# Kernel optimization log

Hardware: AMD Instinct MI355X
Metric: run time of the kernel (lower is better)

Reference implementation:

```python
import jax, jax.numpy as jnp
import numpy as np

B, IN_DIM, HID, LAT, L, K = 65536, 512, 256, 64, 3, 2048


def setup_inputs() -> dict:
    key = jax.random.key(0)
    ks = jax.random.split(key, 10)
    s = 0.05
    return {
        "x": jax.random.normal(ks[0], (B, IN_DIM), jnp.float32),
        "enc_w1": jax.random.normal(ks[1], (IN_DIM, HID), jnp.float32) * s,
        "enc_b1": jnp.zeros((HID,), jnp.float32),
        "enc_w2": jax.random.normal(ks[2], (HID, LAT), jnp.float32) * s,
        "enc_b2": jnp.zeros((LAT,), jnp.float32),
        "codebooks": jax.random.normal(ks[3], (L, K, LAT), jnp.float32),
        "dec_w1": jax.random.normal(ks[4], (LAT, HID), jnp.float32) * s,
        "dec_b1": jnp.zeros((HID,), jnp.float32),
        "dec_w2": jax.random.normal(ks[5], (HID, IN_DIM), jnp.float32) * s,
        "dec_b2": jnp.zeros((IN_DIM,), jnp.float32),
    }


def reference(x, enc_w1, enc_b1, enc_w2, enc_b2, codebooks,
              dec_w1, dec_b1, dec_w2, dec_b2):
    # encoder: Linear -> ReLU -> Linear
    z = jax.nn.relu(x @ enc_w1 + enc_b1) @ enc_w2 + enc_b2  # [B, LAT]

    quantized = jnp.zeros_like(z)
    codes, residuals = [], []
    num_layers = codebooks.shape[0]
    for i in range(num_layers):  # small fixed layer loop (structurally sequential)
        residual = z - jax.lax.stop_gradient(quantized)  # [B, LAT]
        residuals.append(residual)
        C = codebooks[i]  # [K, LAT]
        # squared euclidean distances (argmin identical to cdist argmin)
        sqdist = (jnp.sum(residual * residual, axis=-1, keepdims=True)
                  - 2.0 * (residual @ C.T)
                  + jnp.sum(C * C, axis=-1))  # [B, K]
        code = jnp.argmin(sqdist, axis=-1)  # [B]
        codes.append(code)
        quantized = C[code] + jax.lax.stop_gradient(quantized)

    # decoder: Linear -> ReLU -> Linear
    x_recon = jax.nn.relu(quantized @ dec_w1 + dec_b1) @ dec_w2 + dec_b2  # [B, IN_DIM]
    return (jnp.stack(codes), x_recon, quantized, jnp.stack(residuals))
```

## Files before the change

kernel.cpp:

```cpp
#include <hip/hip_runtime.h>
#include <float.h>

#define NB      65536
#define IN_DIM  512
#define HID     256
#define LAT     64
#define NLAYERS 3
#define NK      2048
#define DELTA   1e-2f

typedef __attribute__((ext_vector_type(8)))  short s16x8;
typedef __attribute__((ext_vector_type(16))) float fp32x16;

__device__ __forceinline__ unsigned short f2bf(float v) {
  unsigned u = __float_as_uint(v);
  unsigned r = (u + 0x7fffu + ((u >> 16) & 1u)) >> 16;
  return (unsigned short)r;
}
__device__ __forceinline__ float bf2f(unsigned short h) {
  return __uint_as_float((unsigned)h << 16);
}

template<bool RELU>
__global__ __launch_bounds__(256) void gemm_f32(
    const float* __restrict__ A, const float* __restrict__ W,
    const float* __restrict__ bias, float* __restrict__ C,
    int M, int N, int K) {
  __shared__ float As[32][132];
  __shared__ float Bs[32][64];
  const int tid = threadIdx.x;
  const int cg  = tid & 15;
  const int rg  = tid >> 4;
  const int m0  = blockIdx.x * 128;
  const int n0  = blockIdx.y * 64;

  float acc[8][4];
#pragma unroll
  for (int i = 0; i < 8; ++i)
#pragma unroll
    for (int j = 0; j < 4; ++j) acc[i][j] = 0.f;

  for (int k0 = 0; k0 < K; k0 += 32) {
#pragma unroll
    for (int p = 0; p < 4; ++p) {
      int a = tid + p * 256;
      int row = a >> 3, kq = (a & 7) * 4;
      float4 v = *reinterpret_cast<const float4*>(&A[(size_t)(m0 + row) * K + k0 + kq]);
      As[kq + 0][row] = v.x; As[kq + 1][row] = v.y;
      As[kq + 2][row] = v.z; As[kq + 3][row] = v.w;
    }
#pragma unroll
    for (int p = 0; p < 2; ++p) {
      int a = tid + p * 256;
      int kk = a >> 4, nq = (a & 15) * 4;
      *reinterpret_cast<float4*>(&Bs[kk][nq]) =
          *reinterpret_cast<const float4*>(&W[(size_t)(k0 + kk) * N + n0 + nq]);
    }
    __syncthreads();
#pragma unroll
    for (int kk = 0; kk < 32; ++kk) {
      float4 a0 = *reinterpret_cast<const float4*>(&As[kk][rg * 8]);
      float4 a1 = *reinterpret_cast<const float4*>(&As[kk][rg * 8 + 4]);
      float4 b0 = *reinterpret_cast<const float4*>(&Bs[kk][cg * 4]);
      float av[8] = {a0.x, a0.y, a0.z, a0.w, a1.x, a1.y, a1.z, a1.w};
      float bv[4] = {b0.x, b0.y, b0.z, b0.w};
#pragma unroll
      for (int i = 0; i < 8; ++i)
#pragma unroll
        for (int j = 0; j < 4; ++j)
          acc[i][j] = fmaf(av[i], bv[j], acc[i][j]);
    }
    __syncthreads();
  }

  float4 bb = *reinterpret_cast<const float4*>(&bias[n0 + cg * 4]);
  float bv[4] = {bb.x, bb.y, bb.z, bb.w};
#pragma unroll
  for (int i = 0; i < 8; ++i) {
    float vals[4];
#pragma unroll
    for (int j = 0; j < 4; ++j) {
      float v = __fadd_rn(acc[i][j], bv[j]);
      if (RELU) v = fmaxf(v, 0.f);
      vals[j] = v;
    }
    float4 o; o.x = vals[0]; o.y = vals[1]; o.z = vals[2]; o.w = vals[3];
    *reinterpret_cast<float4*>(&C[(size_t)(m0 + rg * 8 + i) * N + n0 + cg * 4]) = o;
  }
}

template<bool RELU>
__global__ __launch_bounds__(256) void gemm128(
    const float* __restrict__ A, const float* __restrict__ W,
    const float* __restrict__ bias, float* __restrict__ C,
    int M, int N, int K) {
  __shared__ float As[16][132];
  __shared__ float Bs[16][132];
  const int tid  = threadIdx.x;
  const int cg   = tid & 15;
  const int rg   = tid >> 4;
  const int sw   = (cg >> 2) & 1;
  const int colA = cg * 8 + sw * 4;
  const int colB = cg * 8 + (sw ^ 1) * 4;
  const int m0   = blockIdx.x * 128;
  const int n0   = blockIdx.y * 128;

  const int arow = tid >> 2;
  const int akq  = (tid & 3) * 4;
  const int bk   = tid >> 5;
  const int bn   = (tid & 31) * 4;

  const float* Ap0 = A + (size_t)(m0 + arow) * K + akq;
  const float* Ap1 = A + (size_t)(m0 + arow + 64) * K + akq;
  const float* Wp0 = W + (size_t)bk * N + n0 + bn;
  const float* Wp1 = W + (size_t)(bk + 8) * N + n0 + bn;

  float acc[8][8];
#pragma unroll
  for (int i = 0; i < 8; ++i)
#pragma unroll
    for (int j = 0; j < 8; ++j) acc[i][j] = 0.f;

  float4 av0, av1, bv0, bv1;
  av0 = *reinterpret_cast<const float4*>(Ap0);
  av1 = *reinterpret_cast<const float4*>(Ap1);
  bv0 = *reinterpret_cast<const float4*>(Wp0);
  bv1 = *reinterpret_cast<const float4*>(Wp1);

  auto write_tile = [&]() {
    As[akq + 0][arow] = av0.x; As[akq + 1][arow] = av0.y;
    As[akq + 2][arow] = av0.z; As[akq + 3][arow] = av0.w;
    As[akq + 0][arow + 64] = av1.x; As[akq + 1][arow + 64] = av1.y;
    As[akq + 2][arow + 64] = av1.z; As[akq + 3][arow + 64] = av1.w;
    *reinterpret_cast<float4*>(&Bs[bk][bn])     = bv0;
    *reinterpret_cast<float4*>(&Bs[bk + 8][bn]) = bv1;
  };
  auto compute_tile = [&]() {
#pragma unroll
    for (int kk = 0; kk < 16; ++kk) {
      float4 a0 = *reinterpret_cast<const float4*>(&As[kk][rg * 8]);
      float4 a1 = *reinterpret_cast<const float4*>(&As[kk][rg * 8 + 4]);
      float4 b0 = *reinterpret_cast<const float4*>(&Bs[kk][colA]);
      float4 b1 = *reinterpret_cast<const float4*>(&Bs[kk][colB]);
      float rv[8] = {a0.x, a0.y, a0.z, a0.w, a1.x, a1.y, a1.z, a1.w};
      float cv[8] = {b0.x, b0.y, b0.z, b0.w, b1.x, b1.y, b1.z, b1.w};
#pragma unroll
      for (int i = 0; i < 8; ++i)
#pragma unroll
        for (int j = 0; j < 8; ++j)
          acc[i][j] = fmaf(rv[i], cv[j], acc[i][j]);
    }
  };

  write_tile();
  __syncthreads();
#pragma unroll 1
  for (int k0 = 16; k0 < K; k0 += 16) {
    av0 = *reinterpret_cast<const float4*>(Ap0 + k0);
    av1 = *reinterpret_cast<const float4*>(Ap1 + k0);
    bv0 = *reinterpret_cast<const float4*>(Wp0 + (size_t)k0 * N);
    bv1 = *reinterpret_cast<const float4*>(Wp1 + (size_t)k0 * N);
    compute_tile();
    __syncthreads();
    write_tile();
    __syncthreads();
  }
  compute_tile();

  float4 bA = *reinterpret_cast<const float4*>(&bias[n0 + colA]);
  float4 bB = *reinterpret_cast<const float4*>(&bias[n0 + colB]);
  float ba[8] = {bA.x, bA.y, bA.z, bA.w, bB.x, bB.y, bB.z, bB.w};
#pragma unroll
  for (int i = 0; i < 8; ++i) {
    size_t row = (size_t)(m0 + rg * 8 + i);
    float o[8];
#pragma unroll
    for (int j = 0; j < 8; ++j) {
      float v = __fadd_rn(acc[i][j], ba[j]);
      if (RELU) v = fmaxf(v, 0.f);
      o[j] = v;
    }
    float4 oA; oA.x = o[0]; oA.y = o[1]; oA.z = o[2]; oA.w = o[3];
    float4 oB; oB.x = o[4]; oB.y = o[5]; oB.z = o[6]; oB.w = o[7];
    *reinterpret_cast<float4*>(&C[row * N + n0 + colA]) = oA;
    *reinterpret_cast<float4*>(&C[row * N + n0 + colB]) = oB;
  }
}

__global__ void cnorm_f32(const float* __restrict__ cb, float* __restrict__ cn) {
  int i = blockIdx.x * blockDim.x + threadIdx.x;
  if (i >= NLAYERS * NK) return;
  const float* row = cb + (size_t)i * LAT;
  float r[8];
#pragma unroll
  for (int j = 0; j < 8; ++j) r[j] = 0.f;
#pragma unroll
  for (int t = 0; t < 8; ++t)
#pragma unroll
    for (int j = 0; j < 8; ++j) {
      float v = row[t * 8 + j];
      r[j] = __fadd_rn(r[j], __fmul_rn(v, v));
    }
  cn[i] = __fadd_rn(__fadd_rn(__fadd_rn(r[0], r[1]), __fadd_rn(r[2], r[3])),
                    __fadd_rn(__fadd_rn(r[4], r[5]), __fadd_rn(r[6], r[7])));
}

__global__ void split_cb(const float* __restrict__ cb,
                         unsigned short* __restrict__ cbf) {
  const int sid  = blockIdx.x * 256 + threadIdx.x;
  const int lane = sid & 63;
  const int grp  = sid >> 6;
  const int fg   = grp & 7;
  const int chl  = grp >> 3;
  const int nt = fg >> 2, ks = fg & 3;
  const int layer = chl >> 5, ch = chl & 31;
  const int code = ch * 64 + nt * 32 + (lane & 31);
  const int k0 = ks * 16 + (lane >> 5) * 8;
  const float* src = cb + ((size_t)layer * NK + code) * LAT + k0;
  float4 a = *(const float4*)src;
  float4 b = *(const float4*)(src + 4);
  float v[8] = {a.x, a.y, a.z, a.w, b.x, b.y, b.z, b.w};
  s16x8 hi, lo;
#pragma unroll
  for (int i = 0; i < 8; ++i) {
    float nv = __fmul_rn(-2.f, v[i]);
    unsigned short h = f2bf(nv);
    hi[i] = (short)h;
    lo[i] = (short)f2bf(__fsub_rn(nv, bf2f(h)));
  }
  *(s16x8*)(cbf + ((size_t)grp * 2 + 0) * 512 + lane * 8) = hi;
  *(s16x8*)(cbf + ((size_t)grp * 2 + 1) * 512 + lane * 8) = lo;
}

__global__ void split_w(const float* __restrict__ W,
                        unsigned short* __restrict__ wf, int K, int N) {
  const int total = (K / 16) * (N / 32) * 64;
  const int idx = blockIdx.x * 256 + threadIdx.x;
  if (idx >= total) return;
  const int lane = idx & 63;
  const int grp  = idx >> 6;
  const int ntn  = N / 32;
  const int ks   = grp / ntn;
  const int ntg  = grp % ntn;
  const int col  = ntg * 32 + (lane & 31);
  const int k0   = ks * 16 + (lane >> 5) * 8;
  s16x8 hi, lo;
#pragma unroll
  for (int i = 0; i < 8; ++i) {
    float v = W[(size_t)(k0 + i) * N + col];
    unsigned short h = f2bf(v);
    hi[i] = (short)h;
    lo[i] = (short)f2bf(__fsub_rn(v, bf2f(h)));
  }
  *(s16x8*)(wf + ((size_t)grp * 2 + 0) * 512 + lane * 8) = hi;
  *(s16x8*)(wf + ((size_t)grp * 2 + 1) * 512 + lane * 8) = lo;
}

__global__ __launch_bounds__(256, 2) void rq_mfma(
    const float* __restrict__ zg,
    const float* __restrict__ cb,
    const unsigned short* __restrict__ cbf,
    const float* __restrict__ cnorm,
    float* __restrict__ out_codes,
    float* __restrict__ out_quant,
    float* __restrict__ out_res) {
  __shared__ float m1S[128][2];
  __shared__ int   candS[128][8];
  __shared__ int   cntS[128][2];
  __shared__ int   flagS[128][2];
  __shared__ int   selS[128];
  __shared__ float rnS[128];
  __shared__ float bestD[256];
  __shared__ int   bestK[256];

  const int tid   = threadIdx.x;
  const int w     = tid >> 6;
  const int rgrp  = w >> 1;
  const int chalf = w & 1;
  const int lane  = tid & 63;
  const int half  = lane >> 5;
  const int lcol  = lane & 31;
  const int rb0   = blockIdx.x * 128;

  s16x8 ah[2][4], al[2][4];

  for (int layer = 0; layer < NLAYERS; ++layer) {
    const float* cbL = cb + (size_t)layer * NK * LAT;
    const float* cnL = cnorm + (size_t)layer * NK;
    const unsigned short* cbfL = cbf + (size_t)layer * (NK * LAT * 2);
    float* resL = out_res + (size_t)layer * NB * LAT;

#pragma unroll
    for (int m = 0; m < 2; ++m) {
      const size_t row = (size_t)(rb0 + rgrp * 64 + m * 32 + lcol);
#pragma unroll
      for (int ks = 0; ks < 4; ++ks) {
        const int k0 = ks * 16 + half * 8;
        const float* zp = zg + row * LAT + k0;
        float4 a = *(const float4*)zp;
        float4 b = *(const float4*)(zp + 4);
        float r[8] = {a.x, a.y, a.z, a.w, b.x, b.y, b.z, b.w};
        if (layer > 0) {
          const float* qp = out_quant + row * LAT + k0;
          float4 qa = *(const float4*)qp;
          float4 qb = *(const float4*)(qp + 4);
          float q[8] = {qa.x, qa.y, qa.z, qa.w, qb.x, qb.y, qb.z, qb.w};
#pragma unroll
          for (int i = 0; i < 8; ++i) r[i] = __fsub_rn(r[i], q[i]);
          if (chalf == 0) {
            float4 o0 = {r[0], r[1], r[2], r[3]};
            float4 o1 = {r[4], r[5], r[6], r[7]};
            *(float4*)(resL + row * LAT + k0) = o0;
            *(float4*)(resL + row * LAT + k0 + 4) = o1;
          }
        }
#pragma unroll
        for (int i = 0; i < 8; ++i) {
          unsigned short hh = f2bf(r[i]);
          float hf = bf2f(hh);
          ah[m][ks][i] = (short)hh;
          al[m][ks][i] = (short)f2bf(__fsub_rn(r[i], hf));
        }
      }
    }
    __syncthreads();

    if (tid < 128) {
      const float* rp = resL + (size_t)(rb0 + tid) * LAT;
      float r8[8] = {0.f, 0.f, 0.f, 0.f, 0.f, 0.f, 0.f, 0.f};
#pragma unroll
      for (int tb = 0; tb < 8; ++tb) {
        float4 x0 = *(const float4*)(rp + tb * 8);
        float4 x1 = *(const float4*)(rp + tb * 8 + 4);
        float v[8] = {x0.x, x0.y, x0.z, x0.w, x1.x, x1.y, x1.z, x1.w};
#pragma unroll
        for (int j = 0; j < 8; ++j)
          r8[j] = __fadd_rn(r8[j], __fmul_rn(v[j], v[j]));
      }
      rnS[tid] = __fadd_rn(
          __fadd_rn(__fadd_rn(r8[0], r8[1]), __fadd_rn(r8[2], r8[3])),
          __fadd_rn(__fadd_rn(r8[4], r8[5]), __fadd_rn(r8[6], r8[7])));
    }
    __syncthreads();

    float v1[2][16], v2[2][16];
    int   i1[2][16];
#pragma unroll
    for (int m = 0; m < 2; ++m)
#pragma unroll
      for (int r = 0; r < 16; ++r) {
        v1[m][r] = FLT_MAX; v2[m][r] = FLT_MAX; i1[m][r] = 0;
      }

#pragma unroll 1
    for (int ch = 0; ch < 16; ++ch) {
      const int chg = chalf * 16 + ch;
      const unsigned short* cf = cbfL + (size_t)chg * 8192;
#pragma unroll
      for (int nt = 0; nt < 2; ++nt) {
        const int kbase = chg * 64 + nt * 32 + lcol;
        const float cnv = cnL[kbase];
        s16x8 bh[4], bl[4];
#pragma unroll
        for (int ks = 0; ks < 4; ++ks) {
          bh[ks] = *(const s16x8*)(cf + ((size_t)((nt * 4 + ks) * 2 + 0) * 64 + lane) * 8);
          bl[ks] = *(const s16x8*)(cf + ((size_t)((nt * 4 + ks) * 2 + 1) * 64 + lane) * 8);
        }
        fp32x16 acc0, acc1;
#pragma unroll
        for (int r = 0; r < 16; ++r) { acc0[r] = 0.f; acc1[r] = 0.f; }
#pragma unroll
        for (int ks = 0; ks < 4; ++ks) {
          acc0 = __builtin_amdgcn_mfma_f32_32x32x16_bf16(ah[0][ks], bh[ks], acc0, 0, 0, 0);
          acc1 = __builtin_amdgcn_mfma_f32_32x32x16_bf16(ah[1][ks], bh[ks], acc1, 0, 0, 0);
          acc0 = __builtin_amdgcn_mfma_f32_32x32x16_bf16(ah[0][ks], bl[ks], acc0, 0, 0, 0);
          acc1 = __builtin_amdgcn_mfma_f32_32x32x16_bf16(ah[1][ks], bl[ks], acc1, 0, 0, 0);
          acc0 = __builtin_amdgcn_mfma_f32_32x32x16_bf16(al[0][ks], bh[ks], acc0, 0, 0, 0);
          acc1 = __builtin_amdgcn_mfma_f32_32x32x16_bf16(al[1][ks], bh[ks], acc1, 0, 0, 0);
        }
#pragma unroll
        for (int r = 0; r < 16; ++r) {
          {
            float d = __fadd_rn(cnv, acc0[r]);
            v2[0][r] = __builtin_amdgcn_fmed3f(d, v1[0][r], v2[0][r]);
            bool c = d < v1[0][r];
            i1[0][r] = c ? kbase : i1[0][r];
            v1[0][r] = fminf(v1[0][r], d);
          }
          {
            float d = __fadd_rn(cnv, acc1[r]);
            v2[1][r] = __builtin_amdgcn_fmed3f(d, v1[1][r], v2[1][r]);
            bool c = d < v1[1][r];
            i1[1][r] = c ? kbase : i1[1][r];
            v1[1][r] = fminf(v1[1][r], d);
          }
        }
      }
    }

#pragma unroll
    for (int m = 0; m < 2; ++m)
#pragma unroll
      for (int r = 0; r < 16; ++r) {
        float m1 = v1[m][r];
        m1 = fminf(m1, __shfl_xor(m1, 1));
        m1 = fminf(m1, __shfl_xor(m1, 2));
        m1 = fminf(m1, __shfl_xor(m1, 4));
        m1 = fminf(m1, __shfl_xor(m1, 8));
        m1 = fminf(m1, __shfl_xor(m1, 16));
        const int rowloc = rgrp * 64 + m * 32 + (r & 3) + 8 * (r >> 2) + 4 * half;
        if (lcol == 0) m1S[rowloc][chalf] = m1;
      }
    __syncthreads();
#pragma unroll
    for (int m = 0; m < 2; ++m)
#pragma unroll
      for (int r = 0; r < 16; ++r) {
        const int rowloc = rgrp * 64 + m * 32 + (r & 3) + 8 * (r >> 2) + 4 * half;
        float thr = fminf(m1S[rowloc][0], m1S[rowloc][1]) + DELTA;
        unsigned long long bc = __ballot(v1[m][r] <= thr);
        unsigned long long bf = __ballot(v2[m][r] <= thr);
        unsigned mc = (unsigned)(bc >> (half * 32));
        unsigned mf = (unsigned)(bf >> (half * 32));
        int pos = __popc(mc & ((1u << lcol) - 1u));
        if (v1[m][r] <= thr && pos < 4) candS[rowloc][chalf * 4 + pos] = i1[m][r];
        if (lcol == 0) {
          int c = __popc(mc);
          cntS[rowloc][chalf]  = (c < 4) ? c : 4;
          flagS[rowloc][chalf] = (mf != 0u) || (c > 4);
        }
      }
    __syncthreads();

    if (tid < 128) {
      const int t = tid;
      if ((flagS[t][0] | flagS[t][1]) == 0) {
        const float* rp = resL + (size_t)(rb0 + t) * LAT;
        float rr[64];
#pragma unroll
        for (int j = 0; j < 16; ++j) {
          float4 x = *(const float4*)(rp + j * 4);
          rr[j * 4 + 0] = x.x; rr[j * 4 + 1] = x.y;
          rr[j * 4 + 2] = x.z; rr[j * 4 + 3] = x.w;
        }
        const float rn = rnS[t];
        float bd = FLT_MAX; int bk = 0x7fffffff;
        const int c0 = cntS[t][0], c1n = cntS[t][1];
        for (int c = 0; c < c0 + c1n; ++c) {
          int k = candS[t][(c < c0) ? c : (4 + c - c0)];
          const float* cp = cbL + (size_t)k * LAT;
          float dot = 0.f;
#pragma unroll
          for (int j = 0; j < 64; ++j) dot = fmaf(rr[j], cp[j], dot);
          float d = __fadd_rn(__fsub_rn(rn, __fmul_rn(2.f, dot)), cnL[k]);
          if (d < bd || (d == bd && k < bk)) { bd = d; bk = k; }
        }
        selS[t] = bk;
        out_codes[(size_t)layer * NB + rb0 + t] = (float)bk;
      }
    }
    __syncthreads();

#pragma unroll 1
    for (int t2 = 0; t2 < 128; ++t2) {
      if ((flagS[t2][0] | flagS[t2][1]) == 0) continue;
      const float* rp = resL + (size_t)(rb0 + t2) * LAT;
      const float rn = rnS[t2];
      float bd = FLT_MAX; int bk = 0x7fffffff;
#pragma unroll 1
      for (int j = 0; j < 8; ++j) {
        int k = tid * 8 + j;
        const float* cp = cbL + (size_t)k * LAT;
        float dot = 0.f;
        for (int q = 0; q < 64; ++q) dot = fmaf(rp[q], cp[q], dot);
        float d = __fadd_rn(__fsub_rn(rn, __fmul_rn(2.f, dot)), cnL[k]);
        if (d < bd || (d == bd && k < bk)) { bd = d; bk = k; }
      }
      bestD[tid] = bd; bestK[tid] = bk;
      __syncthreads();
      if (tid == 0) {
        float gd = FLT_MAX; int gk = 0x7fffffff;
        for (int i = 0; i < 256; ++i) {
          float d = bestD[i]; int k = bestK[i];
          if (d < gd || (d == gd && k < gk)) { gd = d; gk = k; }
        }
        selS[t2] = gk;
        out_codes[(size_t)layer * NB + rb0 + t2] = (float)gk;
      }
      __syncthreads();
    }

    if (chalf == 0) {
#pragma unroll
      for (int m = 0; m < 2; ++m) {
        const int rowloc = rgrp * 64 + m * 32 + lcol;
        const size_t row = (size_t)(rb0 + rowloc);
        const int sel = selS[rowloc];
        const float* cp = cbL + (size_t)sel * LAT;
#pragma unroll
        for (int ks = 0; ks < 4; ++ks) {
          const int k0 = ks * 16 + half * 8;
          float4 c0 = *(const float4*)(cp + k0);
          float4 c1 = *(const float4*)(cp + k0 + 4);
          float* qp = out_quant + row * LAT + k0;
          if (layer == 0) {
            *(float4*)qp = c0; *(float4*)(qp + 4) = c1;
          } else {
            float4 q0 = *(const float4*)qp;
            float4 q1 = *(const float4*)(qp + 4);
            q0.x = __fadd_rn(c0.x, q0.x); q0.y = __fadd_rn(c0.y, q0.y);
            q0.z = __fadd_rn(c0.z, q0.z); q0.w = __fadd_rn(c0.w, q0.w);
            q1.x = __fadd_rn(c1.x, q1.x); q1.y = __fadd_rn(c1.y, q1.y);
            q1.z = __fadd_rn(c1.z, q1.z); q1.w = __fadd_rn(c1.w, q1.w);
            *(float4*)qp = q0; *(float4*)(qp + 4) = q1;
          }
        }
      }
    }
    __syncthreads();
  }
}

__global__ __launch_bounds__(256) void dec1_mfma(
    const float* __restrict__ q, const unsigned short* __restrict__ wf,
    const float* __restrict__ bias,
    unsigned short* __restrict__ h_hi, unsigned short* __restrict__ h_lo) {
  const int tid  = threadIdx.x;
  const int w    = tid >> 6;
  const int lane = tid & 63;
  const int half = lane >> 5;
  const int lcol = lane & 31;
  const int m0   = blockIdx.x * 128 + w * 32;
  const int n0   = blockIdx.y * 128;

  fp32x16 acc[4];
#pragma unroll
  for (int nt = 0; nt < 4; ++nt)
#pragma unroll
    for (int r = 0; r < 16; ++r) acc[nt][r] = 0.f;

  const size_t arow = (size_t)(m0 + lcol);
#pragma unroll
  for (int ks = 0; ks < 4; ++ks) {
    const float* ap = q + arow * LAT + ks * 16 + half * 8;
    float4 a0 = *(const float4*)ap;
    float4 a1 = *(const float4*)(ap + 4);
    float av[8] = {a0.x, a0.y, a0.z, a0.w, a1.x, a1.y, a1.z, a1.w};
    s16x8 ah, al;
#pragma unroll
    for (int i = 0; i < 8; ++i) {
      unsigned short hh = f2bf(av[i]);
      ah[i] = (short)hh;
      al[i] = (short)f2bf(__fsub_rn(av[i], bf2f(hh)));
    }
#pragma unroll
    for (int nt = 0; nt < 4; ++nt) {
      const int grp = ks * 8 + (blockIdx.y * 4 + nt);
      const unsigned short* base = wf + (size_t)grp * 1024;
      s16x8 bh = *(const s16x8*)(base + lane * 8);
      s16x8 bl = *(const s16x8*)(base + 512 + lane * 8);
      acc[nt] = __builtin_amdgcn_mfma_f32_32x32x16_bf16(ah, bh, acc[nt], 0, 0, 0);
      acc[nt] = __builtin_amdgcn_mfma_f32_32x32x16_bf16(ah, bl, acc[nt], 0, 0, 0);
      acc[nt] = __builtin_amdgcn_mfma_f32_32x32x16_bf16(al, bh, acc[nt], 0, 0, 0);
    }
  }

#pragma unroll
  for (int nt = 0; nt < 4; ++nt) {
    const int col = n0 + nt * 32 + lcol;
    const float b = bias[col];
#pragma unroll
    for (int r = 0; r < 16; ++r) {
      const int rowo = (r & 3) + 8 * (r >> 2) + 4 * half;
      const size_t grow = (size_t)(m0 + rowo);
      float v = fmaxf(__fadd_rn(acc[nt][r], b), 0.f);
      unsigned short hh = f2bf(v);
      h_hi[grow * HID + col] = hh;
      h_lo[grow * HID + col] = f2bf(__fsub_rn(v, bf2f(hh)));
    }
  }
}

__global__ __launch_bounds__(256) void dec2_mfma(
    const unsigned short* __restrict__ h_hi,
    const unsigned short* __restrict__ h_lo,
    const unsigned short* __restrict__ wf,
    const float* __restrict__ bias, float* __restrict__ C) {
  const int tid  = threadIdx.x;
  const int w    = tid >> 6;
  const int lane = tid & 63;
  const int half = lane >> 5;
  const int lcol = lane & 31;
  const int m0   = blockIdx.x * 128 + w * 32;
  const int n0   = blockIdx.y * 128;

  fp32x16 acc[4];
#pragma unroll
  for (int nt = 0; nt < 4; ++nt)
#pragma unroll
    for (int r = 0; r < 16; ++r) acc[nt][r] = 0.f;

  const size_t arow = (size_t)(m0 + lcol);
#pragma unroll 1
  for (int ks = 0; ks < 16; ++ks) {
    const size_t aoff = arow * HID + ks * 16 + half * 8;
    s16x8 ah = *(const s16x8*)(h_hi + aoff);
    s16x8 al = *(const s16x8*)(h_lo + aoff);
#pragma unroll
    for (int nt = 0; nt < 4; ++nt) {
      const int grp = ks * 16 + (blockIdx.y * 4 + nt);
      const unsigned short* base = wf + (size_t)grp * 1024;
      s16x8 bh = *(const s16x8*)(base + lane * 8);
      s16x8 bl = *(const s16x8*)(base + 512 + lane * 8);
      acc[nt] = __builtin_amdgcn_mfma_f32_32x32x16_bf16(ah, bh, acc[nt], 0, 0, 0);
      acc[nt] = __builtin_amdgcn_mfma_f32_32x32x16_bf16(ah, bl, acc[nt], 0, 0, 0);
      acc[nt] = __builtin_amdgcn_mfma_f32_32x32x16_bf16(al, bh, acc[nt], 0, 0, 0);
    }
  }

#pragma unroll
  for (int nt = 0; nt < 4; ++nt) {
    const int col = n0 + nt * 32 + lcol;
    const float b = bias[col];
#pragma unroll
    for (int r = 0; r < 16; ++r) {
      const int rowo = (r & 3) + 8 * (r >> 2) + 4 * half;
      C[(size_t)(m0 + rowo) * IN_DIM + col] = __fadd_rn(acc[nt][r], b);
    }
  }
}

extern "C" void kernel_launch(void* const* d_in, const int* in_sizes, int n_in,
                              void* d_out, int out_size, void* d_ws, size_t ws_size,
                              hipStream_t stream) {
  (void)in_sizes; (void)n_in; (void)out_size;
  const float* x   = (const float*)d_in[0];
  const float* ew1 = (const float*)d_in[1];
  const float* eb1 = (const float*)d_in[2];
  const float* ew2 = (const float*)d_in[3];
  const float* eb2 = (const float*)d_in[4];
  const float* cbk = (const float*)d_in[5];
  const float* dw1 = (const float*)d_in[6];
  const float* db1 = (const float*)d_in[7];
  const float* dw2 = (const float*)d_in[8];
  const float* db2 = (const float*)d_in[9];

  float* out     = (float*)d_out;
  float* o_codes = out;
  float* o_xrec  = out + (size_t)NLAYERS * NB;
  float* o_quant = o_xrec + (size_t)NB * IN_DIM;
  float* o_res   = o_quant + (size_t)NB * LAT;

  char* ws = (char*)d_ws;
  float* h            = (float*)ws;
  unsigned short* hhi = (unsigned short*)ws;
  unsigned short* hlo = (unsigned short*)(ws + (size_t)32 * 1024 * 1024);
  float* cn           = (float*)(ws + (size_t)64 * 1024 * 1024);
  unsigned short* w1f = (unsigned short*)(ws + (size_t)64 * 1024 * 1024 + 32768);
  unsigned short* w2f = (unsigned short*)(ws + (size_t)64 * 1024 * 1024 + 32768 + 65536);
  const size_t ws_need = (size_t)64 * 1024 * 1024 + 32768 + 65536 + 524288;
  const bool fast_dec = ws_size >= ws_need;

  unsigned short* cbf = (unsigned short*)(o_xrec + (size_t)16 * 1024 * 1024);

  cnorm_f32<<<(NLAYERS * NK + 255) / 256, 256, 0, stream>>>(cbk, cn);
  split_cb<<<192, 256, 0, stream>>>(cbk, cbf);
  if (fast_dec) {
    split_w<<<((LAT / 16) * (HID / 32) * 64 + 255) / 256, 256, 0, stream>>>(dw1, w1f, LAT, HID);
    split_w<<<((HID / 16) * (IN_DIM / 32) * 64 + 255) / 256, 256, 0, stream>>>(dw2, w2f, HID, IN_DIM);
  }
  gemm128<true ><<<dim3(NB / 128, HID / 128), 256, 0, stream>>>(x, ew1, eb1, h,     NB, HID, IN_DIM);
  gemm_f32<false><<<dim3(NB / 128, LAT / 64),  256, 0, stream>>>(h, ew2, eb2, o_res, NB, LAT, HID);
  rq_mfma<<<NB / 128, 256, 0, stream>>>(o_res, cbk, cbf, cn, o_codes, o_quant, o_res);
  if (fast_dec) {
    dec1_mfma<<<dim3(NB / 128, 2), 256, 0, stream>>>(o_quant, w1f, db1, hhi, hlo);
    dec2_mfma<<<dim3(NB / 128, 4), 256, 0, stream>>>(hhi, hlo, w2f, db2, o_xrec);
  } else {
    gemm128<true ><<<dim3(NB / 128, HID / 128),    256, 0, stream>>>(o_quant, dw1, db1, h,      NB, HID,    LAT);
    gemm128<false><<<dim3(NB / 128, IN_DIM / 128), 256, 0, stream>>>(h,       dw2, db2, o_xrec, NB, IN_DIM, HID);
  }
}
```

Before: 733.4 us.

## Halve rq_mfma rows per block and split MFMA accumulators for occupancy

Each rq_mfma block now handles 64 rows instead of 128, so each wave holds one 32-row A fragment instead of two, and the launch bound rises to 3 blocks per CU. The three split-bf16 MFMA products move into two independent accumulators (hi*hi and the cross terms) that are summed before the distance update. This lowers register pressure to raise occupancy, but codebook fragments are now reused across half as many rows, doubling B-fragment global loads per row. The grid also doubles, and the serial fallback loop over flagged rows is shorter per block.

```diff
diff --git a/kernel.cpp b/kernel.cpp
--- a/kernel.cpp
+++ b/kernel.cpp
@@ -256,7 +256,7 @@
   *(s16x8*)(wf + ((size_t)grp * 2 + 1) * 512 + lane * 8) = lo;
 }
 
-__global__ __launch_bounds__(256, 2) void rq_mfma(
+__global__ __launch_bounds__(256, 3) void rq_mfma(
     const float* __restrict__ zg,
     const float* __restrict__ cb,
     const unsigned short* __restrict__ cbf,
@@ -264,25 +264,29 @@
     float* __restrict__ out_codes,
     float* __restrict__ out_quant,
     float* __restrict__ out_res) {
-  __shared__ float m1S[128][2];
-  __shared__ int   candS[128][8];
-  __shared__ int   cntS[128][2];
-  __shared__ int   flagS[128][2];
-  __shared__ int   selS[128];
-  __shared__ float rnS[128];
+  __shared__ float m1S[64][2];
+  __shared__ int   candS[64][8];
+  __shared__ int   cntS[64][2];
+  __shared__ int   flagS[64][2];
+  __shared__ int   selS[64];
+  __shared__ float rnS[64];
   __shared__ float bestD[256];
   __shared__ int   bestK[256];
 
   const int tid   = threadIdx.x;
   const int w     = tid >> 6;
-  const int rgrp  = w >> 1;
+  const int msb   = w >> 1;
   const int chalf = w & 1;
   const int lane  = tid & 63;
   const int half  = lane >> 5;
   const int lcol  = lane & 31;
-  const int rb0   = blockIdx.x * 128;
-
-  s16x8 ah[2][4], al[2][4];
+  const int rb0   = blockIdx.x * 64;
+
+  s16x8 ah[4], al[4];
+
+  fp32x16 Z;
+#pragma unroll
+  for (int r = 0; r < 16; ++r) Z[r] = 0.f;
 
   for (int layer = 0; layer < NLAYERS; ++layer) {
     const float* cbL = cb + (size_t)layer * NK * LAT;
@@ -290,9 +294,8 @@
     const unsigned short* cbfL = cbf + (size_t)layer * (NK * LAT * 2);
     float* resL = out_res + (size_t)layer * NB * LAT;
 
-#pragma unroll
-    for (int m = 0; m < 2; ++m) {
-      const size_t row = (size_t)(rb0 + rgrp * 64 + m * 32 + lcol);
+    {
+      const size_t row = (size_t)(rb0 + msb * 32 + lcol);
 #pragma unroll
       for (int ks = 0; ks < 4; ++ks) {
         const int k0 = ks * 16 + half * 8;
@@ -306,7 +309,7 @@
           float4 qb = *(const float4*)(qp + 4);
           float q[8] = {qa.x, qa.y, qa.z, qa.w, qb.x, qb.y, qb.z, qb.w};
 #pragma unroll
-          for (int i = 0; i < 8; ++i) r[i] = __fsub_rn(r[i], q[i]);
+        for (int i = 0; i < 8; ++i) r[i] = __fsub_rn(r[i], q[i]);
           if (chalf == 0) {
             float4 o0 = {r[0], r[1], r[2], r[3]};
             float4 o1 = {r[4], r[5], r[6], r[7]};
@@ -318,14 +321,14 @@
         for (int i = 0; i < 8; ++i) {
           unsigned short hh = f2bf(r[i]);
           float hf = bf2f(hh);
-          ah[m][ks][i] = (short)hh;
-          al[m][ks][i] = (short)f2bf(__fsub_rn(r[i], hf));
-        }
-      }
-    }
-    __syncthreads();
-
-    if (tid < 128) {
+          ah[ks][i] = (short)hh;
+          al[ks][i] = (short)f2bf(__fsub_rn(r[i], hf));
+        }
+      }
+    }
+    __syncthreads();
+
+    if (tid < 64) {
       const float* rp = resL + (size_t)(rb0 + tid) * LAT;
       float r8[8] = {0.f, 0.f, 0.f, 0.f, 0.f, 0.f, 0.f, 0.f};
 #pragma unroll
@@ -343,14 +346,12 @@
     }
     __syncthreads();
 
-    float v1[2][16], v2[2][16];
-    int   i1[2][16];
-#pragma unroll
-    for (int m = 0; m < 2; ++m)
-#pragma unroll
-      for (int r = 0; r < 16; ++r) {
-        v1[m][r] = FLT_MAX; v2[m][r] = FLT_MAX; i1[m][r] = 0;
-      }
+    float v1[16], v2[16];
+    int   i1[16];
+#pragma unroll
+    for (int r = 0; r < 16; ++r) {
+      v1[r] = FLT_MAX; v2[r] = FLT_MAX; i1[r] = 0;
+    }
 
 #pragma unroll 1
     for (int ch = 0; ch < 16; ++ch) {
@@ -366,73 +367,57 @@
           bh[ks] = *(const s16x8*)(cf + ((size_t)((nt * 4 + ks) * 2 + 0) * 64 + lane) * 8);
           bl[ks] = *(const s16x8*)(cf + ((size_t)((nt * 4 + ks) * 2 + 1) * 64 + lane) * 8);
         }
-        fp32x16 acc0, acc1;
-#pragma unroll
-        for (int r = 0; r < 16; ++r) { acc0[r] = 0.f; acc1[r] = 0.f; }
+        fp32x16 aA = Z, aB = Z;
+#pragma unroll
+        for (int ks = 0; ks < 4; ++ks)
+          aA = __builtin_amdgcn_mfma_f32_32x32x16_bf16(ah[ks], bh[ks], aA, 0, 0, 0);
 #pragma unroll
         for (int ks = 0; ks < 4; ++ks) {
-          acc0 = __builtin_amdgcn_mfma_f32_32x32x16_bf16(ah[0][ks], bh[ks], acc0, 0, 0, 0);
-          acc1 = __builtin_amdgcn_mfma_f32_32x32x16_bf16(ah[1][ks], bh[ks], acc1, 0, 0, 0);
-          acc0 = __builtin_amdgcn_mfma_f32_32x32x16_bf16(ah[0][ks], bl[ks], acc0, 0, 0, 0);
-          acc1 = __builtin_amdgcn_mfma_f32_32x32x16_bf16(ah[1][ks], bl[ks], acc1, 0, 0, 0);
-          acc0 = __builtin_amdgcn_mfma_f32_32x32x16_bf16(al[0][ks], bh[ks], acc0, 0, 0, 0);
-          acc1 = __builtin_amdgcn_mfma_f32_32x32x16_bf16(al[1][ks], bh[ks], acc1, 0, 0, 0);
+          aB = __builtin_amdgcn_mfma_f32_32x32x16_bf16(ah[ks], bl[ks], aB, 0, 0, 0);
+          aB = __builtin_amdgcn_mfma_f32_32x32x16_bf16(al[ks], bh[ks], aB, 0, 0, 0);
         }
 #pragma unroll
         for (int r = 0; r < 16; ++r) {
-          {
-            float d = __fadd_rn(cnv, acc0[r]);
-            v2[0][r] = __builtin_amdgcn_fmed3f(d, v1[0][r], v2[0][r]);
-            bool c = d < v1[0][r];
-            i1[0][r] = c ? kbase : i1[0][r];
-            v1[0][r] = fminf(v1[0][r], d);
-          }
-          {
-            float d = __fadd_rn(cnv, acc1[r]);
-            v2[1][r] = __builtin_amdgcn_fmed3f(d, v1[1][r], v2[1][r]);
-            bool c = d < v1[1][r];
-            i1[1][r] = c ? kbase : i1[1][r];
-            v1[1][r] = fminf(v1[1][r], d);
-          }
-        }
-      }
-    }
-
-#pragma unroll
-    for (int m = 0; m < 2; ++m)
-#pragma unroll
-      for (int r = 0; r < 16; ++r) {
-        float m1 = v1[m][r];
-        m1 = fminf(m1, __shfl_xor(m1, 1));
-        m1 = fminf(m1, __shfl_xor(m1, 2));
-        m1 = fminf(m1, __shfl_xor(m1, 4));
-        m1 = fminf(m1, __shfl_xor(m1, 8));
-        m1 = fminf(m1, __shfl_xor(m1, 16));
-        const int rowloc = rgrp * 64 + m * 32 + (r & 3) + 8 * (r >> 2) + 4 * half;
-        if (lcol == 0) m1S[rowloc][chalf] = m1;
-      }
-    __syncthreads();
-#pragma unroll
-    for (int m = 0; m < 2; ++m)
-#pragma unroll
-      for (int r = 0; r < 16; ++r) {
-        const int rowloc = rgrp * 64 + m * 32 + (r & 3) + 8 * (r >> 2) + 4 * half;
-        float thr = fminf(m1S[rowloc][0], m1S[rowloc][1]) + DELTA;
-        unsigned long long bc = __ballot(v1[m][r] <= thr);
-        unsigned long long bf = __ballot(v2[m][r] <= thr);
-        unsigned mc = (unsigned)(bc >> (half * 32));
-        unsigned mf = (unsigned)(bf >> (half * 32));
-        int pos = __popc(mc & ((1u << lcol) - 1u));
-        if (v1[m][r] <= thr && pos < 4) candS[rowloc][chalf * 4 + pos] = i1[m][r];
-        if (lcol == 0) {
-          int c = __popc(mc);
-          cntS[rowloc][chalf]  = (c < 4) ? c : 4;
-          flagS[rowloc][chalf] = (mf != 0u) || (c > 4);
-        }
-      }
-    __syncthreads();
-
-    if (tid < 128) {
+          float d = __fadd_rn(cnv, __fadd_rn(aA[r], aB[r]));
+          v2[r] = __builtin_amdgcn_fmed3f(d, v1[r], v2[r]);
+          bool c = d < v1[r];
+          i1[r] = c ? kbase : i1[r];
+          v1[r] = fminf(v1[r], d);
+        }
+      }
+    }
+
+#pragma unroll
+    for (int r = 0; r < 16; ++r) {
+      float m1 = v1[r];
+      m1 = fminf(m1, __shfl_xor(m1, 1));
+      m1 = fminf(m1, __shfl_xor(m1, 2));
+      m1 = fminf(m1, __shfl_xor(m1, 4));
+      m1 = fminf(m1, __shfl_xor(m1, 8));
+      m1 = fminf(m1, __shfl_xor(m1, 16));
+      const int rowloc = msb * 32 + (r & 3) + 8 * (r >> 2) + 4 * half;
+      if (lcol == 0) m1S[rowloc][chalf] = m1;
+    }
+    __syncthreads();
+#pragma unroll
+    for (int r = 0; r < 16; ++r) {
+      const int rowloc = msb * 32 + (r & 3) + 8 * (r >> 2) + 4 * half;
+      float thr = fminf(m1S[rowloc][0], m1S[rowloc][1]) + DELTA;
+      unsigned long long bc = __ballot(v1[r] <= thr);
+      unsigned long long bf = __ballot(v2[r] <= thr);
+      unsigned mc = (unsigned)(bc >> (half * 32));
+      unsigned mf = (unsigned)(bf >> (half * 32));
+      int pos = __popc(mc & ((1u << lcol) - 1u));
+      if (v1[r] <= thr && pos < 4) candS[rowloc][chalf * 4 + pos] = i1[r];
+      if (lcol == 0) {
+        int c = __popc(mc);
+        cntS[rowloc][chalf]  = (c < 4) ? c : 4;
+        flagS[rowloc][chalf] = (mf != 0u) || (c > 4);
+      }
+    }
+    __syncthreads();
+
+    if (tid < 64) {
       const int t = tid;
       if ((flagS[t][0] | flagS[t][1]) == 0) {
         const float* rp = resL + (size_t)(rb0 + t) * LAT;
@@ -462,7 +447,7 @@
     __syncthreads();
 
 #pragma unroll 1
-    for (int t2 = 0; t2 < 128; ++t2) {
+    for (int t2 = 0; t2 < 64; ++t2) {
       if ((flagS[t2][0] | flagS[t2][1]) == 0) continue;
       const float* rp = resL + (size_t)(rb0 + t2) * LAT;
       const float rn = rnS[t2];
@@ -491,29 +476,26 @@
     }
 
     if (chalf == 0) {
-#pragma unroll
-      for (int m = 0; m < 2; ++m) {
-        const int rowloc = rgrp * 64 + m * 32 + lcol;
-        const size_t row = (size_t)(rb0 + rowloc);
-        const int sel = selS[rowloc];
-        const float* cp = cbL + (size_t)sel * LAT;
-#pragma unroll
-        for (int ks = 0; ks < 4; ++ks) {
-          const int k0 = ks * 16 + half * 8;
-          float4 c0 = *(const float4*)(cp + k0);
-          float4 c1 = *(const float4*)(cp + k0 + 4);
-          float* qp = out_quant + row * LAT + k0;
-          if (layer == 0) {
-            *(float4*)qp = c0; *(float4*)(qp + 4) = c1;
-          } else {
-            float4 q0 = *(const float4*)qp;
-            float4 q1 = *(const float4*)(qp + 4);
-            q0.x = __fadd_rn(c0.x, q0.x); q0.y = __fadd_rn(c0.y, q0.y);
-            q0.z = __fadd_rn(c0.z, q0.z); q0.w = __fadd_rn(c0.w, q0.w);
-            q1.x = __fadd_rn(c1.x, q1.x); q1.y = __fadd_rn(c1.y, q1.y);
-            q1.z = __fadd_rn(c1.z, q1.z); q1.w = __fadd_rn(c1.w, q1.w);
-            *(float4*)qp = q0; *(float4*)(qp + 4) = q1;
-          }
+      const int rowloc = msb * 32 + lcol;
+      const size_t row = (size_t)(rb0 + rowloc);
+      const int sel = selS[rowloc];
+      const float* cp = cbL + (size_t)sel * LAT;
+#pragma unroll
+      for (int ks = 0; ks < 4; ++ks) {
+        const int k0 = ks * 16 + half * 8;
+        float4 c0 = *(const float4*)(cp + k0);
+        float4 c1 = *(const float4*)(cp + k0 + 4);
+        float* qp = out_quant + row * LAT + k0;
+        if (layer == 0) {
+          *(float4*)qp = c0; *(float4*)(qp + 4) = c1;
+        } else {
+          float4 q0 = *(const float4*)qp;
+          float4 q1 = *(const float4*)(qp + 4);
+          q0.x = __fadd_rn(c0.x, q0.x); q0.y = __fadd_rn(c0.y, q0.y);
+          q0.z = __fadd_rn(c0.z, q0.z); q0.w = __fadd_rn(c0.w, q0.w);
+          q1.x = __fadd_rn(c1.x, q1.x); q1.y = __fadd_rn(c1.y, q1.y);
+          q1.z = __fadd_rn(c1.z, q1.z); q1.w = __fadd_rn(c1.w, q1.w);
+          *(float4*)qp = q0; *(float4*)(qp + 4) = q1;
         }
       }
     }
@@ -671,7 +653,7 @@
   }
   gemm128<true ><<<dim3(NB / 128, HID / 128), 256, 0, stream>>>(x, ew1, eb1, h,     NB, HID, IN_DIM);
   gemm_f32<false><<<dim3(NB / 128, LAT / 64),  256, 0, stream>>>(h, ew2, eb2, o_res, NB, LAT, HID);
-  rq_mfma<<<NB / 128, 256, 0, stream>>>(o_res, cbk, cbf, cn, o_codes, o_quant, o_res);
+  rq_mfma<<<NB / 64, 256, 0, stream>>>(o_res, cbk, cbf, cn, o_codes, o_quant, o_res);
   if (fast_dec) {
     dec1_mfma<<<dim3(NB / 128, 2), 256, 0, stream>>>(o_quant, w1f, db1, hhi, hlo);
     dec2_mfma<<<dim3(NB / 128, 4), 256, 0, stream>>>(hhi, hlo, w2f, db2, o_xrec);
```

After: 866.6 us. 18.2% more time.
